# Kernel optimization log

Measured on AMD Instinct MI355X. Metric: run time of the kernel, lower is better.

The kernel has to match this reference:

```python
import jax, jax.numpy as jnp
import numpy as np

H = 16  # num_heads


def setup_inputs() -> dict:
    key = jax.random.key(0)
    ks = jax.random.split(key, 12)
    B, S, D = 2, 2048, 1024
    init = lambda k, shape: (jax.random.normal(k, shape, dtype=jnp.float32) * 0.02)
    return {
        "x": jax.random.normal(ks[0], (B, S, D), dtype=jnp.float32),
        "wq": init(ks[1], (D, D)), "bq": init(ks[2], (D,)),
        "wk": init(ks[3], (D, D)), "bk": init(ks[4], (D,)),
        "wv": init(ks[5], (D, D)), "bv": init(ks[6], (D,)),
        "wo": init(ks[7], (D, D)), "bo": init(ks[8], (D,)),
        "w3d": init(ks[9], (3, D)), "b3d": init(ks[10], (3,)),
    }


def _pairwise_l2(pos):
    # pos: [B,S,3] -> [B,S,S] Euclidean distance (safe sqrt: zero grad at 0, like torch.cdist)
    sq = jnp.sum((pos[:, :, None, :] - pos[:, None, :, :]) ** 2, axis=-1)
    safe = jnp.where(sq > 0, sq, 1.0)
    return jnp.where(sq > 0, jnp.sqrt(safe), 0.0)


def reference(x, wq, bq, wk, bk, wv, bv, wo, bo, w3d, b3d):
    B, S, D = x.shape
    hd = D // H
    scale = 1.0 / (hd ** 0.5)
    # V projection -> [B,H,S,hd]  (Q/K are computed in torch forward but unused in APPROX scores)
    V = (x @ wv.T + bv).reshape(B, S, H, hd).transpose(0, 2, 1, 3)
    # 3D semantic positions and non-dot-product scores (identical across heads)
    pos = x @ w3d.T + b3d                      # [B,S,3]
    dist = _pairwise_l2(pos)                   # [B,S,S]
    scores = -dist[:, None, :, :] * scale      # [B,H,S,S] (broadcast over heads)
    causal = jnp.triu(jnp.ones((S, S), dtype=bool), k=1)
    scores = jnp.where(causal[None, None], -jnp.inf, scores)
    attn = jax.nn.softmax(scores, axis=-1)
    attn = jnp.nan_to_num(attn, nan=0.0)
    out = jnp.einsum('bhqk,bhkd->bhqd', attn, V)  # [B,H,S,hd]
    out = out.transpose(0, 2, 1, 3).reshape(B, S, D)
    return out @ wo.T + bo
```

## Files before the change

kernel.cpp:

```cpp
#include <hip/hip_runtime.h>
#include <hip/hip_bf16.h>
#include <stdint.h>


typedef __attribute__((ext_vector_type(8))) short bf16x8;
typedef __attribute__((ext_vector_type(4))) float f32x4;
typedef __attribute__((ext_vector_type(4))) unsigned short us4;

#define AS1(p) (const __attribute__((address_space(1))) unsigned int*)(p)
#define AS3(p) (__attribute__((address_space(3))) unsigned int*)(p)

__device__ __forceinline__ unsigned short f2bf(float f) {
  union { float f; unsigned u; } v; v.f = f;
  unsigned r = v.u + 0x7FFFu + ((v.u >> 16) & 1u);
  return (unsigned short)(r >> 16);
}

__global__ void k_pos(const float* __restrict__ x, const float* __restrict__ w3d,
                      const float* __restrict__ b3d, float* __restrict__ pos) {
  __shared__ float red[12];
  const int row = blockIdx.x, t = threadIdx.x;
  const float4 xv = ((const float4*)(x + (size_t)row * 1024))[t];
  const float4 w0 = ((const float4*)(w3d))[t];
  const float4 w1 = ((const float4*)(w3d + 1024))[t];
  const float4 w2 = ((const float4*)(w3d + 2048))[t];
  float a0 = xv.x*w0.x + xv.y*w0.y + xv.z*w0.z + xv.w*w0.w;
  float a1 = xv.x*w1.x + xv.y*w1.y + xv.z*w1.z + xv.w*w1.w;
  float a2 = xv.x*w2.x + xv.y*w2.y + xv.z*w2.z + xv.w*w2.w;
  #pragma unroll
  for (int off = 32; off; off >>= 1) {
    a0 += __shfl_down(a0, off, 64);
    a1 += __shfl_down(a1, off, 64);
    a2 += __shfl_down(a2, off, 64);
  }
  if ((t & 63) == 0) { red[(t >> 6)*3] = a0; red[(t >> 6)*3 + 1] = a1; red[(t >> 6)*3 + 2] = a2; }
  __syncthreads();
  if (t == 0) {
    pos[(size_t)row*3 + 0] = red[0] + red[3] + red[6] + red[9]  + b3d[0];
    pos[(size_t)row*3 + 1] = red[1] + red[4] + red[7] + red[10] + b3d[1];
    pos[(size_t)row*3 + 2] = red[2] + red[5] + red[8] + red[11] + b3d[2];
  }
}

__global__ void k_fused(const float* __restrict__ x, const float* __restrict__ wv,
                        const float* __restrict__ wo, const float* __restrict__ bv,
                        const float* __restrict__ bo, const float* __restrict__ pos,
                        unsigned short* __restrict__ xT, unsigned short* __restrict__ wvT,
                        unsigned short* __restrict__ wob, float* __restrict__ cvec,
                        unsigned short* __restrict__ Ab) {
  __shared__ __align__(16) float lsm[64 * 68];
  const int bx = blockIdx.x, t = threadIdx.x;
  if (bx < 1024) {
    const int b = bx >> 9, rest = bx & 511, st = rest >> 4, dt = rest & 15;
    const int s0 = st * 64, d0 = dt * 64;
    const int r = t >> 2, c4 = t & 3;
    const float* src = x + (size_t)(b * 2048 + s0 + r) * 1024 + d0;
    float (*ld)[68] = (float(*)[68])lsm;
    #pragma unroll
    for (int p = 0; p < 4; p++)
      *(float4*)&ld[r][(c4 + 4 * p) * 4] = ((const float4*)src)[c4 + 4 * p];
    __syncthreads();
    #pragma unroll
    for (int p = 0; p < 4; p++) {
      const int dl = (t >> 4) + (p << 4);
      us4 o;
      #pragma unroll
      for (int k = 0; k < 4; k++)
        ((unsigned short*)&o)[k] = f2bf(ld[(t & 15) * 4 + k][dl]);
      *(us4*)(xT + ((size_t)b << 21) + (size_t)(d0 + dl) * 2048 + s0 + (t & 15) * 4) = o;
    }
  } else if (bx < 2048) {
    const int bb = bx - 1024, tr = bb >> 5, tc = bb & 31;
    const int r = t >> 5, c = t & 31;
    float (*ld)[33] = (float(*)[33])lsm;
    #pragma unroll
    for (int rr = r; rr < 32; rr += 8)
      ld[rr][c] = wv[(size_t)(tr * 32 + rr) * 1024 + tc * 32 + c];
    __syncthreads();
    #pragma unroll
    for (int rr = r; rr < 32; rr += 8)
      wvT[(size_t)(tc * 32 + rr) * 1024 + tr * 32 + c] = f2bf(ld[c][rr]);
  } else if (bx < 3072) {
    const int oo = bx - 2048;
    const float4 w = ((const float4*)(wo + (size_t)oo * 1024))[t];
    us4 ob; ob.x = f2bf(w.x); ob.y = f2bf(w.y); ob.z = f2bf(w.z); ob.w = f2bf(w.w);
    ((us4*)(wob + (size_t)oo * 1024))[t] = ob;
    const float4 b = ((const float4*)bv)[t];
    float a = w.x * b.x + w.y * b.y + w.z * b.z + w.w * b.w;
    #pragma unroll
    for (int off = 32; off; off >>= 1) a += __shfl_down(a, off, 64);
    if ((t & 63) == 0) lsm[t >> 6] = a;
    __syncthreads();
    if (t == 0) cvec[oo] = lsm[0] + lsm[1] + lsm[2] + lsm[3] + bo[oo];
  } else {
    const int row = bx - 3072;
    const int q = row & 2047, bb = row >> 11;
    const float* pb = pos + ((size_t)bb << 11) * 3;
    const float qx = pb[q*3], qy = pb[q*3+1], qz = pb[q*3+2];
    const float4* pb4 = (const float4*)pb;
    const int jmax = ((q >> 7) + 1) << 7;
    float v[2][4];
    float sum = 0.f;
    #pragma unroll
    for (int cc = 0; cc < 2; cc++) {
      const int j0 = (cc << 10) + (t << 2);
      float e0 = 0.f, e1 = 0.f, e2 = 0.f, e3 = 0.f;
      if (j0 < jmax) {
        const float4 A4 = pb4[3*(j0 >> 2)], B4 = pb4[3*(j0 >> 2) + 1], C4 = pb4[3*(j0 >> 2) + 2];
        const float px[4] = {A4.x, A4.w, B4.z, C4.y};
        const float py[4] = {A4.y, B4.x, B4.w, C4.z};
        const float pz[4] = {A4.z, B4.y, C4.x, C4.w};
        float ee[4];
        #pragma unroll
        for (int u = 0; u < 4; u++) {
          float e = 0.f;
          if (j0 + u <= q) {
            float dx = qx - px[u], dy = qy - py[u], dz = qz - pz[u];
            float sq = fmaf(dx, dx, fmaf(dy, dy, dz*dz));
            float d = sq > 0.f ? sqrtf(sq) : 0.f;
            e = __expf(-0.125f * d);
          }
          ee[u] = e;
        }
        e0 = ee[0]; e1 = ee[1]; e2 = ee[2]; e3 = ee[3];
      }
      v[cc][0] = e0; v[cc][1] = e1; v[cc][2] = e2; v[cc][3] = e3;
      sum += e0 + e1 + e2 + e3;
    }
    #pragma unroll
    for (int off = 32; off; off >>= 1) sum += __shfl_down(sum, off, 64);
    if ((t & 63) == 0) lsm[t >> 6] = sum;
    __syncthreads();
    const float inv = 1.f / (lsm[0] + lsm[1] + lsm[2] + lsm[3]);
    unsigned short* orow = Ab + (size_t)row * 2048;
    #pragma unroll
    for (int cc = 0; cc < 2; cc++) {
      const int j0 = (cc << 10) + (t << 2);
      if (j0 < jmax) {
        us4 o;
        o.x = f2bf(v[cc][0]*inv); o.y = f2bf(v[cc][1]*inv);
        o.z = f2bf(v[cc][2]*inv); o.w = f2bf(v[cc][3]*inv);
        *(us4*)(orow + j0) = o;
      }
    }
  }
}

template<int BM, int BN, int WM, int WN>
__device__ __forceinline__ void gemm_ring(
    const unsigned short* __restrict__ A, int lda,
    const unsigned short* __restrict__ Bt, int ldb,
    int m0, int n0, int kmax,
    unsigned short* lds, f32x4* acc) {
  constexpr int WAVES = WM * WN;
  constexpr int FI = BM / (WM * 16), FJ = BN / (WN * 16);
  constexpr int CPW = ((BM + BN) / 8) / WAVES;
  constexpr int BUFSZ = (BM + BN) * 64;
  const int tid = threadIdx.x, l = tid & 63, w = tid >> 6;
  const int wm = w & (WM - 1), wn = w / WM;
  const int gcol = ((l & 7) ^ (l >> 3)) << 3;

  auto stage = [&](int buf, int k0) {
    unsigned short* base = lds + buf * BUFSZ;
    #pragma unroll
    for (int e = 0; e < CPW; ++e) {
      const int c = w * CPW + e;
      const unsigned short* src;
      unsigned short* dst;
      if (c < BM / 8) {
        src = A + (size_t)(m0 + c*8 + (l >> 3)) * lda + k0 + gcol;
        dst = base + c * 512;
      } else {
        const int cb = c - BM / 8;
        src = Bt + (size_t)(n0 + cb*8 + (l >> 3)) * ldb + k0 + gcol;
        dst = base + BM * 64 + cb * 512;
      }
      __builtin_amdgcn_global_load_lds(AS1(src), AS3(dst), 16, 0, 0);
    }
  };

  auto compute = [&](int buf) {
    unsigned short* lA = lds + buf * BUFSZ;
    unsigned short* lB = lA + BM * 64;
    #pragma unroll
    for (int h = 0; h < 2; ++h) {
      const int slot = ((h << 2) | (l >> 4)) ^ (l & 7);
      bf16x8 af[FI], bfr[FJ];
      #pragma unroll
      for (int i = 0; i < FI; ++i) {
        const int ar = wm * (BM / WM) + i * 16 + (l & 15);
        af[i] = *(const bf16x8*)&lA[ar * 64 + slot * 8];
      }
      #pragma unroll
      for (int j = 0; j < FJ; ++j) {
        const int br = wn * (BN / WN) + j * 16 + (l & 15);
        bfr[j] = *(const bf16x8*)&lB[br * 64 + slot * 8];
      }
      #pragma unroll
      for (int i = 0; i < FI; ++i)
        #pragma unroll
        for (int j = 0; j < FJ; ++j)
          acc[i * FJ + j] = __builtin_amdgcn_mfma_f32_16x16x32_bf16(af[i], bfr[j], acc[i * FJ + j], 0, 0, 0);
    }
  };

  const int NT = kmax >> 6;
  stage(0, 0);
  if (NT > 1) stage(1, 64);
  int cur = 0, nxt2 = 2;
  for (int t = 0; t < NT; ++t) {
    if (t < NT - 1) {
      static_assert(CPW == 4 || CPW == 6 || CPW == 8, "vmcnt literal");
      if constexpr (CPW == 4) asm volatile("s_waitcnt vmcnt(4) lgkmcnt(0)" ::: "memory");
      else if constexpr (CPW == 6) asm volatile("s_waitcnt vmcnt(6) lgkmcnt(0)" ::: "memory");
      else asm volatile("s_waitcnt vmcnt(8) lgkmcnt(0)" ::: "memory");
    } else {
      asm volatile("s_waitcnt vmcnt(0) lgkmcnt(0)" ::: "memory");
    }
    __builtin_amdgcn_s_barrier();
    if (t + 2 < NT) stage(nxt2, (t + 2) << 6);
    compute(cur);
    cur = cur == 2 ? 0 : cur + 1;
    nxt2 = nxt2 == 2 ? 0 : nxt2 + 1;
  }
}

__global__ __launch_bounds__(256, 2) void k_gemm_axwc(
    const unsigned short* __restrict__ Ab, const unsigned short* __restrict__ xT,
    unsigned short* __restrict__ Axb,
    const unsigned short* __restrict__ wob, const unsigned short* __restrict__ wvT,
    unsigned short* __restrict__ Wcs) {
  __shared__ __align__(16) unsigned short lds[3 * (128 + 64) * 64];
  const int bx = blockIdx.x;
  const int l = threadIdx.x & 63, w = threadIdx.x >> 6;
  const int wm = w & 1, wn = w >> 1;
  if (bx < 512) {
    f32x4 acc[8] = {};
    const int xcd = bx & 7, rest = bx >> 3;
    const int g = rest >> 4, n0i = rest & 15;
    const int mi = (g < 2) ? (15 - xcd) : xcd;
    const int b = g & 1;
    const int m0 = mi << 7, n0 = n0i << 6;
    const unsigned short* A  = Ab + ((size_t)b << 22);
    const unsigned short* Bt = xT + ((size_t)b << 21);
    gemm_ring<128, 64, 2, 2>(A, 2048, Bt, 2048, m0, n0, (mi + 1) << 7, lds, acc);
    unsigned short* Obase = Axb + ((size_t)b << 11) * 1024;
    #pragma unroll
    for (int i = 0; i < 4; i++) {
      const int r0 = m0 + wm*64 + i*16 + ((l >> 4) << 2);
      #pragma unroll
      for (int j = 0; j < 2; j++) {
        const int cidx = n0 + wn*32 + j*16 + (l & 15);
        #pragma unroll
        for (int t = 0; t < 4; t++)
          Obase[(size_t)(r0 + t) * 1024 + cidx] = f2bf(acc[i*2 + j][t]);
      }
    }
  } else {
    f32x4 acc[4] = {};
    const int g = bx - 512;
    const int m0 = (g & 15) * 64, n0 = (g >> 4) * 64;
    gemm_ring<64, 64, 2, 2>(wob, 1024, wvT, 1024, m0, n0, 1024, lds, acc);
    #pragma unroll
    for (int i = 0; i < 2; i++) {
      const int r0 = m0 + wm*32 + i*16 + ((l >> 4) << 2);
      #pragma unroll
      for (int j = 0; j < 2; j++) {
        const int cidx = n0 + wn*32 + j*16 + (l & 15);
        #pragma unroll
        for (int t = 0; t < 4; t++)
          Wcs[(size_t)(r0 + t) * 1024 + cidx] = f2bf(acc[i*2 + j][t]);
      }
    }
  }
}

__global__ __launch_bounds__(256, 2) void k_gemm_out(
    const unsigned short* __restrict__ Axb, const unsigned short* __restrict__ Wcs,
    const float* __restrict__ cvec, float* __restrict__ out) {
  __shared__ __align__(16) unsigned short lds[3 * (128 + 64) * 64];
  f32x4 acc[8] = {};
  const int m0 = blockIdx.x * 128, n0 = blockIdx.y * 64;
  gemm_ring<128, 64, 2, 2>(Axb, 1024, Wcs, 1024, m0, n0, 1024, lds, acc);
  const int l = threadIdx.x & 63, w = threadIdx.x >> 6;
  const int wm = w & 1, wn = w >> 1;
  #pragma unroll
  for (int i = 0; i < 4; i++) {
    const int r0 = m0 + wm*64 + i*16 + ((l >> 4) << 2);
    #pragma unroll
    for (int j = 0; j < 2; j++) {
      const int cidx = n0 + wn*32 + j*16 + (l & 15);
      const float cv = cvec[cidx];
      #pragma unroll
      for (int t = 0; t < 4; t++)
        out[(size_t)(r0 + t) * 1024 + cidx] = acc[i*2 + j][t] + cv;
    }
  }
}

extern "C" void kernel_launch(void* const* d_in, const int* in_sizes, int n_in,
                              void* d_out, int out_size, void* d_ws, size_t ws_size,
                              hipStream_t stream) {
  const float* x   = (const float*)d_in[0];
  const float* wv  = (const float*)d_in[5];
  const float* bv  = (const float*)d_in[6];
  const float* wo  = (const float*)d_in[7];
  const float* bo  = (const float*)d_in[8];
  const float* w3d = (const float*)d_in[9];
  const float* b3d = (const float*)d_in[10];
  float* out = (float*)d_out;

  char* ws = (char*)d_ws;
  unsigned short* xT  = (unsigned short*)(ws);
  unsigned short* wvT = (unsigned short*)(ws + ( 8u << 20));
  unsigned short* wob = (unsigned short*)(ws + (10u << 20));
  unsigned short* Wcs = (unsigned short*)(ws + (12u << 20));
  unsigned short* Axb = (unsigned short*)(ws + (14u << 20));
  unsigned short* Ab  = (unsigned short*)(ws + (22u << 20));
  float*          pos = (float*)(ws + (38u << 20));
  float*          cvec= (float*)(ws + (39u << 20));

  k_pos<<<4096, 256, 0, stream>>>(x, w3d, b3d, pos);
  k_fused<<<7168, 256, 0, stream>>>(x, wv, wo, bv, bo, pos, xT, wvT, wob, cvec, Ab);
  k_gemm_axwc<<<768, 256, 0, stream>>>(Ab, xT, Axb, wob, wvT, Wcs);
  k_gemm_out<<<dim3(32, 16), 256, 0, stream>>>(Axb, Wcs, cvec, out);
}
```

Before: 56.78 us.

## Merge output GEMM into producer kernel with atomic work queue and dependency flags

Fuses the A·x / Wc GEMM kernel and the final output GEMM into one persistent-style launch. Blocks take work items from an atomic counter so producers are dispatched before consumers. Each output tile spin-waits on per-row-block and per-column-block completion counters instead of a kernel boundary. This removes one launch and lets output tiles start as soon as their inputs are ready, at the cost of a memset, atomics, and possible spin stalls.

```diff
diff --git a/kernel.cpp b/kernel.cpp
--- a/kernel.cpp
+++ b/kernel.cpp
@@ -225,15 +225,22 @@
   }
 }
 
-__global__ __launch_bounds__(256, 2) void k_gemm_axwc(
+__global__ __launch_bounds__(256, 2) void k_gemm_all(
     const unsigned short* __restrict__ Ab, const unsigned short* __restrict__ xT,
     unsigned short* __restrict__ Axb,
     const unsigned short* __restrict__ wob, const unsigned short* __restrict__ wvT,
-    unsigned short* __restrict__ Wcs) {
+    unsigned short* __restrict__ Wcs, const float* __restrict__ cvec,
+    float* __restrict__ out, unsigned* __restrict__ sync) {
   __shared__ __align__(16) unsigned short lds[3 * (128 + 64) * 64];
-  const int bx = blockIdx.x;
-  const int l = threadIdx.x & 63, w = threadIdx.x >> 6;
+  __shared__ unsigned item_s;
+  const int tid = threadIdx.x;
+  if (tid == 0)
+    item_s = __hip_atomic_fetch_add(&sync[0], 1u, __ATOMIC_RELAXED, __HIP_MEMORY_SCOPE_AGENT);
+  __syncthreads();
+  const int bx = (int)item_s;
+  const int l = tid & 63, w = tid >> 6;
   const int wm = w & 1, wn = w >> 1;
+
   if (bx < 512) {
     f32x4 acc[8] = {};
     const int xcd = bx & 7, rest = bx >> 3;
@@ -256,7 +263,12 @@
           Obase[(size_t)(r0 + t) * 1024 + cidx] = f2bf(acc[i*2 + j][t]);
       }
     }
-  } else {
+    __syncthreads();
+    if (tid == 0) {
+      __threadfence();
+      __hip_atomic_fetch_add(&sync[1 + b*16 + mi], 1u, __ATOMIC_RELEASE, __HIP_MEMORY_SCOPE_AGENT);
+    }
+  } else if (bx < 768) {
     f32x4 acc[4] = {};
     const int g = bx - 512;
     const int m0 = (g & 15) * 64, n0 = (g >> 4) * 64;
@@ -272,28 +284,36 @@
           Wcs[(size_t)(r0 + t) * 1024 + cidx] = f2bf(acc[i*2 + j][t]);
       }
     }
-  }
-}
-
-__global__ __launch_bounds__(256, 2) void k_gemm_out(
-    const unsigned short* __restrict__ Axb, const unsigned short* __restrict__ Wcs,
-    const float* __restrict__ cvec, float* __restrict__ out) {
-  __shared__ __align__(16) unsigned short lds[3 * (128 + 64) * 64];
-  f32x4 acc[8] = {};
-  const int m0 = blockIdx.x * 128, n0 = blockIdx.y * 64;
-  gemm_ring<128, 64, 2, 2>(Axb, 1024, Wcs, 1024, m0, n0, 1024, lds, acc);
-  const int l = threadIdx.x & 63, w = threadIdx.x >> 6;
-  const int wm = w & 1, wn = w >> 1;
-  #pragma unroll
-  for (int i = 0; i < 4; i++) {
-    const int r0 = m0 + wm*64 + i*16 + ((l >> 4) << 2);
-    #pragma unroll
-    for (int j = 0; j < 2; j++) {
-      const int cidx = n0 + wn*32 + j*16 + (l & 15);
-      const float cv = cvec[cidx];
-      #pragma unroll
-      for (int t = 0; t < 4; t++)
-        out[(size_t)(r0 + t) * 1024 + cidx] = acc[i*2 + j][t] + cv;
+    __syncthreads();
+    if (tid == 0) {
+      __threadfence();
+      __hip_atomic_fetch_add(&sync[33 + (g & 15)], 1u, __ATOMIC_RELEASE, __HIP_MEMORY_SCOPE_AGENT);
+    }
+  } else {
+    const int u = bx - 768;
+    const int m = u & 31, n = u >> 5;
+    if (tid == 0) {
+      while (__hip_atomic_load(&sync[1 + m], __ATOMIC_ACQUIRE, __HIP_MEMORY_SCOPE_AGENT) < 16u)
+        __builtin_amdgcn_s_sleep(2);
+      while (__hip_atomic_load(&sync[33 + n], __ATOMIC_ACQUIRE, __HIP_MEMORY_SCOPE_AGENT) < 16u)
+        __builtin_amdgcn_s_sleep(2);
+      __threadfence();
+    }
+    __syncthreads();
+    f32x4 acc[8] = {};
+    const int m0 = m * 128, n0 = n * 64;
+    gemm_ring<128, 64, 2, 2>(Axb, 1024, Wcs, 1024, m0, n0, 1024, lds, acc);
+    #pragma unroll
+    for (int i = 0; i < 4; i++) {
+      const int r0 = m0 + wm*64 + i*16 + ((l >> 4) << 2);
+      #pragma unroll
+      for (int j = 0; j < 2; j++) {
+        const int cidx = n0 + wn*32 + j*16 + (l & 15);
+        const float cv = cvec[cidx];
+        #pragma unroll
+        for (int t = 0; t < 4; t++)
+          out[(size_t)(r0 + t) * 1024 + cidx] = acc[i*2 + j][t] + cv;
+      }
     }
   }
 }
@@ -319,9 +339,10 @@
   unsigned short* Ab  = (unsigned short*)(ws + (22u << 20));
   float*          pos = (float*)(ws + (38u << 20));
   float*          cvec= (float*)(ws + (39u << 20));
-
+  unsigned*       sync= (unsigned*)(ws + (40u << 20));
+
+  hipMemsetAsync(sync, 0, 49 * sizeof(unsigned), stream);
   k_pos<<<4096, 256, 0, stream>>>(x, w3d, b3d, pos);
   k_fused<<<7168, 256, 0, stream>>>(x, wv, wo, bv, bo, pos, xT, wvT, wob, cvec, Ab);
-  k_gemm_axwc<<<768, 256, 0, stream>>>(Ab, xT, Axb, wob, wvT, Wcs);
-  k_gemm_out<<<dim3(32, 16), 256, 0, stream>>>(Axb, Wcs, cvec, out);
-}
+  k_gemm_all<<<1280, 256, 0, stream>>>(Ab, xT, Axb, wob, wvT, Wcs, cvec, out, sync);
+}
```

Result: slower. 205.6 us (+262.0%).
